# Performance work log

Hardware: AMD Instinct MI355X
Metric: run time of the kernel (lower is better)

Reference implementation:

```python
import jax, jax.numpy as jnp
import numpy as np

N = 100000      # nodes
E = 1600000     # directed edges
F_IN = 128      # input features
H = 64          # hidden_channels
C = 32          # num_classes


def setup_inputs() -> dict:
    key = jax.random.key(0)
    ks = jax.random.split(key, 8)
    x = jax.random.normal(ks[0], (N, F_IN), jnp.float32)
    edge_index = jax.random.randint(ks[1], (2, E), 0, N, jnp.int32)
    W1 = jax.random.normal(ks[2], (F_IN, H), jnp.float32) * (1.0 / np.sqrt(F_IN))
    b1 = jnp.zeros((H,), jnp.float32)
    W2 = jax.random.normal(ks[3], (H, H), jnp.float32) * (1.0 / np.sqrt(H))
    b2 = jnp.zeros((H,), jnp.float32)
    Wout = jax.random.normal(ks[4], (H, C), jnp.float32) * (1.0 / np.sqrt(H))
    bout = jnp.zeros((C,), jnp.float32)
    return {"x": x, "edge_index": edge_index, "W1": W1, "b1": b1,
            "W2": W2, "b2": b2, "Wout": Wout, "bout": bout}


def gcn_conv(x, W, b, src, dst, n):
    """PyG GCNConv: out = D^-1/2 (A + I) D^-1/2 (X W) + b,
    with degree computed on A + I."""
    h = x @ W  # [N, out]
    ones = jnp.ones(dst.shape[0], h.dtype)
    deg = jax.ops.segment_sum(ones, dst, num_segments=n) + 1.0  # self-loop
    dinv = jax.lax.rsqrt(deg)                                   # [N]
    coef = dinv[src] * dinv[dst]                                # [E]
    agg = jax.ops.segment_sum(h[src] * coef[:, None], dst, num_segments=n)
    agg = agg + h * (dinv * dinv)[:, None]                      # self-loop message
    return agg + b


def reference(x, edge_index, W1, b1, W2, b2, Wout, bout):
    src, dst = edge_index[0], edge_index[1]
    n = x.shape[0]
    h = jax.nn.relu(gcn_conv(x, W1, b1, src, dst, n))
    # dropout(p=0.5) is a no-op in eval mode
    h = jax.nn.relu(gcn_conv(h, W2, b2, src, dst, n))
    return jax.nn.softmax(h @ Wout + bout, axis=1)
```

## Files before the change

kernel.cpp:

```cpp
#include <hip/hip_runtime.h>
#include <stdint.h>


typedef unsigned short u16;
typedef unsigned int u32;
typedef unsigned long long u64t;
typedef __attribute__((ext_vector_type(8))) short bf16x8;
typedef __attribute__((ext_vector_type(4))) float f32x4;

#define GN 100000
#define GE 1600000
#define NBKT 196
#define BCAP 10240
#define EBLK 782
#define B24 16777216
#define QSC 1048576.0f
#define QIV 9.5367431640625e-7f

__device__ __forceinline__ float bf2f(u32 lo16) {
  union { u32 i; float f; } v; v.i = lo16 << 16; return v.f;
}
__device__ __forceinline__ u16 f2bf(float f) {
  union { float f; u32 i; } v; v.f = f;
  u32 x = v.i;
  u32 r = x + 0x7fffu + ((x >> 16) & 1u);
  return (u16)(r >> 16);
}
__device__ __forceinline__ u32 pack2(float a, float b) {
  return (u32)f2bf(a) | ((u32)f2bf(b) << 16);
}

__global__ __launch_bounds__(256) void k_detect(const u16* __restrict__ xs,
                                                int* __restrict__ flag,
                                                int* __restrict__ ccount) {
  __shared__ int cnt;
  if (threadIdx.x == 0) cnt = 0;
  if (threadIdx.x < NBKT) ccount[threadIdx.x] = 0;
  __syncthreads();
  int w = 0;
#pragma unroll
  for (int i = 0; i < 16; i++) {
    int s = threadIdx.x * 16 + i;
    u32 u = xs[(size_t)s * 1562];
    u32 ex = (u >> 7) & 0xffu;
    if (ex == 0xffu || ex < 0x40u) w++;
  }
  atomicAdd(&cnt, w);
  __syncthreads();
  if (threadIdx.x == 0) flag[0] = (cnt >= 64) ? 0 : 1;
}

__global__ __launch_bounds__(256) void k_partA(const int* __restrict__ src,
                                               const int* __restrict__ dst,
                                               int* __restrict__ ccount, int E,
                                               const void* p2, const void* p3,
                                               const void* p4, const void* p5,
                                               const void* p6, const void* p7,
                                               const int* __restrict__ flag,
                                               float* __restrict__ Wf,
                                               u16* __restrict__ Wb1,
                                               u16* __restrict__ Wb2,
                                               u16* __restrict__ Wbo,
                                               u32* __restrict__ pairs) {
  int tid = threadIdx.x;
  if (blockIdx.x >= EBLK) {
    int i = (blockIdx.x - EBLK) * 256 + tid;
    bool isbf = flag[0] != 0;
    if (i < 14496) {
      const void* sp; int off;
      if (i < 8192)       { sp = p2; off = i; }
      else if (i < 8256)  { sp = p3; off = i - 8192; }
      else if (i < 12352) { sp = p4; off = i - 8256; }
      else if (i < 12416) { sp = p5; off = i - 12352; }
      else if (i < 14464) { sp = p6; off = i - 12416; }
      else                { sp = p7; off = i - 14464; }
      Wf[i] = isbf ? bf2f((u32)((const u16*)sp)[off]) : ((const float*)sp)[off];
    } else if (i < 14496 + 12288) {
      int idx = i - 14496;
      const void* W; u16* dstp;
      if (idx < 8192) { W = p2; dstp = Wb1; }
      else            { W = p4; dstp = Wb2; idx -= 8192; }
      int j  = idx & 7;
      int l  = (idx >> 3) & 63;
      int c  = (idx >> 9) & 3;
      int kc = idx >> 11;
      int k = kc * 32 + (l >> 4) * 8 + j;
      int n = c * 16 + (l & 15);
      dstp[idx] = isbf ? ((const u16*)W)[k * 64 + n]
                       : f2bf(((const float*)W)[k * 64 + n]);
    } else if (i < 14496 + 12288 + 2048) {
      int idx = i - 14496 - 12288;
      int j  = idx & 7;
      int l  = (idx >> 3) & 63;
      int c  = (idx >> 9) & 1;
      int kc = idx >> 10;
      int k = kc * 32 + (l >> 4) * 8 + j;
      int n = c * 16 + (l & 15);
      Wbo[idx] = isbf ? ((const u16*)p6)[k * 32 + n]
                      : f2bf(((const float*)p6)[k * 32 + n]);
    }
    return;
  }
  __shared__ int hist[256];
  __shared__ int boff[256];
  __shared__ int fill[256];
  __shared__ int gbase[256];
  __shared__ int sc[256];
  __shared__ u32 buf[2048];
  __shared__ int adr[2048];
  __shared__ int stotal;
  hist[tid] = 0;
  __syncthreads();
  int e0 = (blockIdx.x * 256 + tid) * 8;
  int s_[8], d_[8];
  int cnt = 0;
  if (e0 + 8 <= E) {
    const int4* sp = (const int4*)(src + e0);
    const int4* dp = (const int4*)(dst + e0);
#pragma unroll
    for (int q = 0; q < 2; q++) {
      int4 sv = sp[q], dv = dp[q];
      s_[4 * q + 0] = sv.x; s_[4 * q + 1] = sv.y;
      s_[4 * q + 2] = sv.z; s_[4 * q + 3] = sv.w;
      d_[4 * q + 0] = dv.x; d_[4 * q + 1] = dv.y;
      d_[4 * q + 2] = dv.z; d_[4 * q + 3] = dv.w;
    }
    cnt = 8;
  } else {
    for (int q = 0; q < 8 && e0 + q < E; q++) {
      s_[q] = src[e0 + q]; d_[q] = dst[e0 + q]; cnt++;
    }
  }
  for (int q = 0; q < cnt; q++) atomicAdd(&hist[d_[q] >> 9], 1);
  __syncthreads();
  int v = hist[tid];
  sc[tid] = v;
  __syncthreads();
#pragma unroll
  for (int off = 1; off < 256; off <<= 1) {
    int a = (tid >= off) ? sc[tid - off] : 0;
    __syncthreads();
    sc[tid] += a;
    __syncthreads();
  }
  int excl = sc[tid] - v;
  boff[tid] = excl;
  fill[tid] = excl;
  if (tid == 255) stotal = sc[255];
  if (tid < NBKT && v > 0) gbase[tid] = tid * BCAP + atomicAdd(&ccount[tid], v);
  __syncthreads();
  for (int q = 0; q < cnt; q++) {
    int bkt = d_[q] >> 9;
    int p = atomicAdd(&fill[bkt], 1);
    buf[p] = ((u32)s_[q] << 9) | ((u32)d_[q] & 511u);
    adr[p] = gbase[bkt] + (p - boff[bkt]);
  }
  __syncthreads();
  int total = stotal;
  for (int j = tid; j < total; j += 256) pairs[adr[j]] = buf[j];
}

__global__ __launch_bounds__(256) void k_partBsrc(u32* __restrict__ pairs,
                                                  const int* __restrict__ ccount,
                                                  int* __restrict__ deg, int N) {
  __shared__ u32 P[BCAP];
  __shared__ u32 S[BCAP];
  __shared__ int cnt[512];
  __shared__ int sh[256];
  __shared__ int sc[256];
  int b = blockIdx.x, tid = threadIdx.x;
  int beg = b * BCAP, m = ccount[b];
  cnt[tid] = 0; cnt[tid + 256] = 0; sh[tid] = 0;
  for (int i = tid; i < m; i += 256) P[i] = pairs[beg + i];
  __syncthreads();
  for (int i = tid; i < m; i += 256) {
    u32 p = P[i];
    atomicAdd(&cnt[p & 511u], 1);
    atomicAdd(&sh[p >> 18], 1);
  }
  __syncthreads();
  int v = sh[tid];
  sc[tid] = v;
  __syncthreads();
#pragma unroll
  for (int off = 1; off < 256; off <<= 1) {
    int a = (tid >= off) ? sc[tid - off] : 0;
    __syncthreads();
    sc[tid] += a;
    __syncthreads();
  }
  __syncthreads();
  sh[tid] = sc[tid] - v;
  __syncthreads();
  for (int i = tid; i < m; i += 256) {
    u32 p = P[i];
    int pos = atomicAdd(&sh[p >> 18], 1);
    S[pos] = p;
  }
  __syncthreads();
  for (int i = tid; i < m; i += 256) pairs[beg + i] = S[i];
  int n0 = (b << 9) + tid, n1 = n0 + 256;
  if (n0 < N) deg[n0] = cnt[tid];
  if (n1 < N) deg[n1] = cnt[tid + 256];
}

template <int K, int XMODE>
__global__ __launch_bounds__(256) void k_mgemm(const void* __restrict__ X,
                                               const u16* __restrict__ Wb,
                                               const int* __restrict__ deg,
                                               const int* __restrict__ flag,
                                               u16* __restrict__ out, int M) {
  constexpr int NKC = K / 32;
  constexpr int P = K + 8;
  __shared__ u16 Bs[NKC * 4 * 64 * 8];
  __shared__ u16 As[128 * P];
  int tid = threadIdx.x;
  bool isbf = (XMODE == 1) ? true : (flag[0] != 0);
#pragma unroll
  for (int i = 0; i < NKC; i++)
    ((uint4*)Bs)[i * 256 + tid] = ((const uint4*)Wb)[i * 256 + tid];

  int rowbase = blockIdx.x * 128;
  int rowsValid = M - rowbase; if (rowsValid > 128) rowsValid = 128;
  if (isbf) {
    constexpr int F8 = K / 8;
    constexpr int NL = K / 16;
    const uint4* Xg = (const uint4*)X;
    uint4 v[NL];
#pragma unroll
    for (int i = 0; i < NL; i++) {
      int q = i * 256 + tid;
      int row = q / F8, c8 = q % F8;
      v[i] = (row < rowsValid) ? Xg[(size_t)(rowbase + row) * F8 + c8]
                               : make_uint4(0, 0, 0, 0);
    }
#pragma unroll
    for (int i = 0; i < NL; i++) {
      int q = i * 256 + tid;
      int row = q / F8, c8 = q % F8;
      *(uint4*)&As[row * P + c8 * 8] = v[i];
    }
  } else {
    constexpr int F4 = K / 4;
    constexpr int NL = K / 8;
    const float4* Xg = (const float4*)X;
    float4 v[NL];
#pragma unroll
    for (int i = 0; i < NL; i++) {
      int q = i * 256 + tid;
      int row = q / F4, c4 = q % F4;
      v[i] = (row < rowsValid) ? Xg[(size_t)(rowbase + row) * F4 + c4]
                               : make_float4(0.f, 0.f, 0.f, 0.f);
    }
#pragma unroll
    for (int i = 0; i < NL; i++) {
      int q = i * 256 + tid;
      int row = q / F4, c4 = q % F4;
      u32* d = (u32*)&As[row * P + c4 * 4];
      d[0] = pack2(v[i].x, v[i].y);
      d[1] = pack2(v[i].z, v[i].w);
    }
  }
  __syncthreads();

  int lane = tid & 63, wave = tid >> 6;
  int m0 = lane & 15;
  int koff = (lane >> 4) * 8;
  f32x4 acc[2][4];
#pragma unroll
  for (int t = 0; t < 2; t++)
#pragma unroll
    for (int c = 0; c < 4; c++) acc[t][c] = (f32x4){0.f, 0.f, 0.f, 0.f};

#pragma unroll
  for (int kc = 0; kc < NKC; kc++) {
    union { uint4 v; bf16x8 s; } a[2];
#pragma unroll
    for (int t = 0; t < 2; t++) {
      int rl = wave * 32 + t * 16 + m0;
      a[t].v = *(const uint4*)&As[rl * P + kc * 32 + koff];
    }
#pragma unroll
    for (int c = 0; c < 4; c++) {
      bf16x8 b = *(const bf16x8*)&Bs[((kc * 4 + c) * 64 + lane) * 8];
      acc[0][c] = __builtin_amdgcn_mfma_f32_16x16x32_bf16(a[0].s, b, acc[0][c], 0, 0, 0);
      acc[1][c] = __builtin_amdgcn_mfma_f32_16x16x32_bf16(a[1].s, b, acc[1][c], 0, 0, 0);
    }
  }
  __syncthreads();
  int cl = lane & 15, rq = (lane >> 4) * 4;
#pragma unroll
  for (int t = 0; t < 2; t++)
#pragma unroll
    for (int reg = 0; reg < 4; reg++) {
      int rl = wave * 32 + t * 16 + rq + reg;
      int r = rowbase + rl;
      float s = (r < M) ? rsqrtf((float)deg[r] + 1.0f) : 0.f;
#pragma unroll
      for (int c = 0; c < 4; c++)
        As[rl * P + c * 16 + cl] = f2bf(acc[t][c][reg] * s);
    }
  __syncthreads();
  uint4* outg = (uint4*)out;
#pragma unroll
  for (int i = 0; i < 4; i++) {
    int q = i * 256 + tid;
    int row = q >> 3, c8 = q & 7;
    int r = rowbase + row;
    if (r < M) outg[(size_t)r * 8 + c8] = *(uint4*)&As[row * P + c8 * 8];
  }
}

template <int MODE>
__global__ __launch_bounds__(1024) void k_aggu(const u16* __restrict__ g,
                                               const u32* __restrict__ pairs,
                                               const int* __restrict__ ccount,
                                               const float* __restrict__ bias,
                                               const u16* __restrict__ Wfrag,
                                               const float* __restrict__ bof,
                                               const int* __restrict__ flag,
                                               void* __restrict__ outv) {
  __shared__ __align__(16) u64t accU[512 * 33];
  __shared__ int cntE[512];
  u16* T16 = (u16*)accU;
  int tid = threadIdx.x;
  int b = blockIdx.x;
  for (int i = tid; i < 512 * 33; i += 1024) accU[i] = 0ull;
  if (tid < 512) cntE[tid] = 0;
  __syncthreads();

  int beg = b * BCAP;
  int end = beg + ccount[b];
  int o = tid >> 3, fq = tid & 7;
  const uint4* gp4 = (const uint4*)g;

#define DSU(dlo, v)                                                          \
  do {                                                                       \
    u64t* rp_ = &accU[(int)(dlo) * 33 + fq * 4];                             \
    int q0_ = (int)(bf2f((v).x & 0xffffu) * QSC) + B24;                      \
    int q1_ = (int)(bf2f((v).x >> 16) * QSC) + B24;                          \
    int q2_ = (int)(bf2f((v).y & 0xffffu) * QSC) + B24;                      \
    int q3_ = (int)(bf2f((v).y >> 16) * QSC) + B24;                          \
    int q4_ = (int)(bf2f((v).z & 0xffffu) * QSC) + B24;                      \
    int q5_ = (int)(bf2f((v).z >> 16) * QSC) + B24;                          \
    int q6_ = (int)(bf2f((v).w & 0xffffu) * QSC) + B24;                      \
    int q7_ = (int)(bf2f((v).w >> 16) * QSC) + B24;                          \
    atomicAdd(rp_ + 0, ((u64t)(u32)q0_) | (((u64t)(u32)q1_) << 32));         \
    atomicAdd(rp_ + 1, ((u64t)(u32)q2_) | (((u64t)(u32)q3_) << 32));         \
    atomicAdd(rp_ + 2, ((u64t)(u32)q4_) | (((u64t)(u32)q5_) << 32));         \
    atomicAdd(rp_ + 3, ((u64t)(u32)q6_) | (((u64t)(u32)q7_) << 32));         \
    if (fq == 0) atomicAdd(&cntE[(int)(dlo)], 1);                            \
  } while (0)

  int e = beg + o;
  for (; e + 384 < end; e += 512) {
    u32 p0 = pairs[e], p1 = pairs[e + 128], p2 = pairs[e + 256], p3 = pairs[e + 384];
    uint4 v0 = gp4[(size_t)(p0 >> 9) * 8 + fq];
    uint4 v1 = gp4[(size_t)(p1 >> 9) * 8 + fq];
    uint4 v2 = gp4[(size_t)(p2 >> 9) * 8 + fq];
    uint4 v3 = gp4[(size_t)(p3 >> 9) * 8 + fq];
    DSU(p0 & 511u, v0); DSU(p1 & 511u, v1);
    DSU(p2 & 511u, v2); DSU(p3 & 511u, v3);
  }
  for (; e < end; e += 128) {
    u32 p = pairs[e];
    uint4 v = gp4[(size_t)(p >> 9) * 8 + fq];
    DSU(p & 511u, v);
  }
#undef DSU
  __syncthreads();

  u32 pk[4][4];
  int rowq[4], c8q[4];
#pragma unroll
  for (int i = 0; i < 4; i++) {
    int q = i * 1024 + tid;
    int row = q >> 3, c8 = q & 7;
    rowq[i] = row; c8q[i] = c8;
    int node = b * 512 + row;
    float f0 = 0.f, f1 = 0.f, f2 = 0.f, f3 = 0.f;
    float f4 = 0.f, f5 = 0.f, f6 = 0.f, f7 = 0.f;
    if (node < GN) {
      uint4 sv = gp4[(size_t)node * 8 + c8];
      int n = cntE[row];
      int nb = n * B24;
      float dv = rsqrtf((float)n + 1.0f);
      float4 b0 = ((const float4*)bias)[c8 * 2];
      float4 b1 = ((const float4*)bias)[c8 * 2 + 1];
      const u64t* up = &accU[row * 33 + c8 * 4];
      u64t w0 = up[0], w1 = up[1], w2 = up[2], w3 = up[3];
      int a0 = (int)((u32)w0) - nb, a1 = (int)((u32)(w0 >> 32)) - nb;
      int a2 = (int)((u32)w1) - nb, a3 = (int)((u32)(w1 >> 32)) - nb;
      int a4 = (int)((u32)w2) - nb, a5 = (int)((u32)(w2 >> 32)) - nb;
      int a6 = (int)((u32)w3) - nb, a7 = (int)((u32)(w3 >> 32)) - nb;
      f0 = fmaxf(dv * ((float)a0 * QIV + bf2f(sv.x & 0xffffu)) + b0.x, 0.f);
      f1 = fmaxf(dv * ((float)a1 * QIV + bf2f(sv.x >> 16))     + b0.y, 0.f);
      f2 = fmaxf(dv * ((float)a2 * QIV + bf2f(sv.y & 0xffffu)) + b0.z, 0.f);
      f3 = fmaxf(dv * ((float)a3 * QIV + bf2f(sv.y >> 16))     + b0.w, 0.f);
      f4 = fmaxf(dv * ((float)a4 * QIV + bf2f(sv.z & 0xffffu)) + b1.x, 0.f);
      f5 = fmaxf(dv * ((float)a5 * QIV + bf2f(sv.z >> 16))     + b1.y, 0.f);
      f6 = fmaxf(dv * ((float)a6 * QIV + bf2f(sv.w & 0xffffu)) + b1.z, 0.f);
      f7 = fmaxf(dv * ((float)a7 * QIV + bf2f(sv.w >> 16))     + b1.w, 0.f);
    }
    pk[i][0] = pack2(f0, f1); pk[i][1] = pack2(f2, f3);
    pk[i][2] = pack2(f4, f5); pk[i][3] = pack2(f6, f7);
  }
  __syncthreads();
#pragma unroll
  for (int i = 0; i < 4; i++)
    *(uint4*)&T16[rowq[i] * 72 + c8q[i] * 8] =
        make_uint4(pk[i][0], pk[i][1], pk[i][2], pk[i][3]);
  __syncthreads();

  int lane = tid & 63, wave = tid >> 6;
  int m0 = lane & 15, koff = (lane >> 4) * 8;
  int cl = lane & 15, rq = (lane >> 4) * 4;
  if (MODE == 0) {
    bf16x8 bfr[2][4];
#pragma unroll
    for (int kc = 0; kc < 2; kc++)
#pragma unroll
      for (int c = 0; c < 4; c++)
        bfr[kc][c] = *(const bf16x8*)&Wfrag[((kc * 4 + c) * 64 + lane) * 8];
    f32x4 acc[2][4];
#pragma unroll
    for (int t = 0; t < 2; t++)
#pragma unroll
      for (int c = 0; c < 4; c++) acc[t][c] = (f32x4){0.f, 0.f, 0.f, 0.f};
#pragma unroll
    for (int kc = 0; kc < 2; kc++) {
      union { uint4 v; bf16x8 s; } a[2];
#pragma unroll
      for (int t = 0; t < 2; t++)
        a[t].v = *(const uint4*)&T16[(wave * 32 + t * 16 + m0) * 72 + kc * 32 + koff];
#pragma unroll
      for (int c = 0; c < 4; c++) {
        acc[0][c] = __builtin_amdgcn_mfma_f32_16x16x32_bf16(a[0].s, bfr[kc][c], acc[0][c], 0, 0, 0);
        acc[1][c] = __builtin_amdgcn_mfma_f32_16x16x32_bf16(a[1].s, bfr[kc][c], acc[1][c], 0, 0, 0);
      }
    }
    __syncthreads();
#pragma unroll
    for (int t = 0; t < 2; t++)
#pragma unroll
      for (int reg = 0; reg < 4; reg++) {
        int rl = wave * 32 + t * 16 + rq + reg;
        int node = b * 512 + rl;
        float s = (node < GN) ? rsqrtf((float)cntE[rl] + 1.0f) : 0.f;
#pragma unroll
        for (int c = 0; c < 4; c++)
          T16[rl * 72 + c * 16 + cl] = f2bf(acc[t][c][reg] * s);
      }
    __syncthreads();
    uint4* og = (uint4*)outv;
#pragma unroll
    for (int i = 0; i < 4; i++) {
      int q = i * 1024 + tid;
      int row = q >> 3, c8 = q & 7;
      int node = b * 512 + row;
      if (node < GN) og[(size_t)node * 8 + c8] = *(uint4*)&T16[row * 72 + c8 * 8];
    }
  } else {
    bf16x8 bfr[2][2];
#pragma unroll
    for (int kc = 0; kc < 2; kc++)
#pragma unroll
      for (int cc = 0; cc < 2; cc++)
        bfr[kc][cc] = *(const bf16x8*)&Wfrag[((kc * 2 + cc) * 64 + lane) * 8];
    f32x4 acc[2][2];
#pragma unroll
    for (int t = 0; t < 2; t++)
#pragma unroll
      for (int c = 0; c < 2; c++) acc[t][c] = (f32x4){0.f, 0.f, 0.f, 0.f};
#pragma unroll
    for (int kc = 0; kc < 2; kc++) {
      union { uint4 v; bf16x8 s; } a[2];
#pragma unroll
      for (int t = 0; t < 2; t++)
        a[t].v = *(const uint4*)&T16[(wave * 32 + t * 16 + m0) * 72 + kc * 32 + koff];
#pragma unroll
      for (int c = 0; c < 2; c++) {
        acc[0][c] = __builtin_amdgcn_mfma_f32_16x16x32_bf16(a[0].s, bfr[kc][c], acc[0][c], 0, 0, 0);
        acc[1][c] = __builtin_amdgcn_mfma_f32_16x16x32_bf16(a[1].s, bfr[kc][c], acc[1][c], 0, 0, 0);
      }
    }
    bool isbf = flag[0] != 0;
    float bb0 = bof[cl], bb1 = bof[16 + cl];
#pragma unroll
    for (int t = 0; t < 2; t++)
#pragma unroll
      for (int reg = 0; reg < 4; reg++) {
        int r = b * 512 + wave * 32 + t * 16 + rq + reg;
        float v0 = acc[t][0][reg] + bb0;
        float v1 = acc[t][1][reg] + bb1;
        float mx = fmaxf(v0, v1);
        mx = fmaxf(mx, __shfl_xor(mx, 1));
        mx = fmaxf(mx, __shfl_xor(mx, 2));
        mx = fmaxf(mx, __shfl_xor(mx, 4));
        mx = fmaxf(mx, __shfl_xor(mx, 8));
        float e0 = __expf(v0 - mx), e1 = __expf(v1 - mx);
        float s = e0 + e1;
        s += __shfl_xor(s, 1);
        s += __shfl_xor(s, 2);
        s += __shfl_xor(s, 4);
        s += __shfl_xor(s, 8);
        float inv = 1.f / s;
        if (r < GN) {
          if (isbf) {
            u16* go = (u16*)outv;
            go[(size_t)r * 32 + cl]      = f2bf(e0 * inv);
            go[(size_t)r * 32 + 16 + cl] = f2bf(e1 * inv);
          } else {
            float* go = (float*)outv;
            go[(size_t)r * 32 + cl]      = e0 * inv;
            go[(size_t)r * 32 + 16 + cl] = e1 * inv;
          }
        }
      }
  }
}

extern "C" void kernel_launch(void* const* d_in, const int* in_sizes, int n_in,
                              void* d_out, int out_size, void* d_ws, size_t ws_size,
                              hipStream_t stream) {
  (void)in_sizes; (void)n_in; (void)out_size; (void)ws_size;
  const void* x  = d_in[0];
  const int* ei  = (const int*)d_in[1];
  const int E = GE;
  const int* srcI = ei;
  const int* dstI = ei + E;

  char* ws = (char*)d_ws;
  int*   flag   = (int*)(ws + 0);
  int*   ccount = (int*)(ws + 256);
  int*   deg    = (int*)(ws + 4096);
  float* Wf     = (float*)(ws + 404480);
  u16*   Wb1    = (u16*)(ws + 462464);
  u16*   Wb2    = (u16*)(ws + 478848);
  u16*   Wbo    = (u16*)(ws + 487040);
  u32*   pairs  = (u32*)(ws + 491520);
  u16*   gA     = (u16*)(ws + 8519680);
  u16*   gB     = (u16*)(ws + 21319680);

  float* b1f = Wf + 8192;
  float* b2f = Wf + 12352;
  float* bof = Wf + 14464;

  k_detect<<<1, 256, 0, stream>>>((const u16*)x, flag, ccount);
  k_partA<<<EBLK + 113, 256, 0, stream>>>(srcI, dstI, ccount, E,
                                          d_in[2], d_in[3], d_in[4], d_in[5],
                                          d_in[6], d_in[7], flag,
                                          Wf, Wb1, Wb2, Wbo, pairs);
  k_partBsrc<<<NBKT, 256, 0, stream>>>(pairs, ccount, deg, GN);
  k_mgemm<128, 0><<<782, 256, 0, stream>>>(x, Wb1, deg, flag, gA, GN);
  k_aggu<0><<<NBKT, 1024, 0, stream>>>(gA, pairs, ccount, b1f, Wb2, bof, flag, gB);
  k_aggu<1><<<NBKT, 1024, 0, stream>>>(gB, pairs, ccount, b2f, Wbo, bof, flag, d_out);
}
```

Before: 226.0 us.

## Sort bucket edges by destination and aggregate contiguous runs in registers

The bucket partition pass now counting-sorts each bucket's edges by local destination instead of by source high bits. The aggregation kernels give each 8-lane group a contiguous chunk of edges and accumulate runs of equal destination in fp32 registers, issuing one set of shared-memory 64-bit atomics per run instead of per edge. This cuts LDS atomic traffic and contention, but trades away source locality in the gather and adds per-thread chunk load imbalance plus branchy run-detection code.

```diff
diff --git a/kernel.cpp b/kernel.cpp
--- a/kernel.cpp
+++ b/kernel.cpp
@@ -7,6 +7,7 @@
 typedef unsigned long long u64t;
 typedef __attribute__((ext_vector_type(8))) short bf16x8;
 typedef __attribute__((ext_vector_type(4))) float f32x4;
+typedef __attribute__((ext_vector_type(2))) float f32x2;
 
 #define GN 100000
 #define GE 1600000
@@ -28,6 +29,11 @@
 }
 __device__ __forceinline__ u32 pack2(float a, float b) {
   return (u32)f2bf(a) | ((u32)f2bf(b) << 16);
+}
+__device__ __forceinline__ f32x2 unpk(u32 u) {
+  union { u32 i; float f; } lo, hi;
+  lo.i = u << 16; hi.i = u & 0xffff0000u;
+  return (f32x2){lo.f, hi.f};
 }
 
 __global__ __launch_bounds__(256) void k_detect(const u16* __restrict__ xs,
@@ -160,27 +166,24 @@
   for (int j = tid; j < total; j += 256) pairs[adr[j]] = buf[j];
 }
 
-__global__ __launch_bounds__(256) void k_partBsrc(u32* __restrict__ pairs,
+__global__ __launch_bounds__(256) void k_partBdlo(u32* __restrict__ pairs,
                                                   const int* __restrict__ ccount,
                                                   int* __restrict__ deg, int N) {
   __shared__ u32 P[BCAP];
   __shared__ u32 S[BCAP];
   __shared__ int cnt[512];
-  __shared__ int sh[256];
   __shared__ int sc[256];
   int b = blockIdx.x, tid = threadIdx.x;
   int beg = b * BCAP, m = ccount[b];
-  cnt[tid] = 0; cnt[tid + 256] = 0; sh[tid] = 0;
+  if (m > BCAP) m = BCAP;
+  cnt[tid] = 0; cnt[tid + 256] = 0;
   for (int i = tid; i < m; i += 256) P[i] = pairs[beg + i];
   __syncthreads();
-  for (int i = tid; i < m; i += 256) {
-    u32 p = P[i];
-    atomicAdd(&cnt[p & 511u], 1);
-    atomicAdd(&sh[p >> 18], 1);
-  }
-  __syncthreads();
-  int v = sh[tid];
-  sc[tid] = v;
+  for (int i = tid; i < m; i += 256) atomicAdd(&cnt[P[i] & 511u], 1);
+  __syncthreads();
+  int c0 = cnt[2 * tid], c1 = cnt[2 * tid + 1];
+  int s = c0 + c1;
+  sc[tid] = s;
   __syncthreads();
 #pragma unroll
   for (int off = 1; off < 256; off <<= 1) {
@@ -189,19 +192,20 @@
     sc[tid] += a;
     __syncthreads();
   }
-  __syncthreads();
-  sh[tid] = sc[tid] - v;
+  int excl = sc[tid] - s;
+  cnt[2 * tid] = excl;
+  cnt[2 * tid + 1] = excl + c0;
+  int n0 = (b << 9) + 2 * tid, n1 = n0 + 1;
+  if (n0 < N) deg[n0] = c0;
+  if (n1 < N) deg[n1] = c1;
   __syncthreads();
   for (int i = tid; i < m; i += 256) {
     u32 p = P[i];
-    int pos = atomicAdd(&sh[p >> 18], 1);
+    int pos = atomicAdd(&cnt[p & 511u], 1);
     S[pos] = p;
   }
   __syncthreads();
   for (int i = tid; i < m; i += 256) pairs[beg + i] = S[i];
-  int n0 = (b << 9) + tid, n1 = n0 + 256;
-  if (n0 < N) deg[n0] = cnt[tid];
-  if (n1 < N) deg[n1] = cnt[tid + 256];
 }
 
 template <int K, int XMODE>
@@ -312,7 +316,7 @@
 }
 
 template <int MODE>
-__global__ __launch_bounds__(1024) void k_aggu(const u16* __restrict__ g,
+__global__ __launch_bounds__(1024) void k_aggr(const u16* __restrict__ g,
                                                const u32* __restrict__ pairs,
                                                const int* __restrict__ ccount,
                                                const float* __restrict__ bias,
@@ -330,44 +334,70 @@
   __syncthreads();
 
   int beg = b * BCAP;
-  int end = beg + ccount[b];
+  int m = ccount[b];
+  if (m > BCAP) m = BCAP;
+  int end = beg + m;
   int o = tid >> 3, fq = tid & 7;
   const uint4* gp4 = (const uint4*)g;
 
-#define DSU(dlo, v)                                                          \
+  int C = (m + 127) >> 7;
+  int lo = beg + o * C;
+  int hi = lo + C; if (hi > end) hi = end;
+
+  f32x2 a0 = {0.f, 0.f}, a1 = {0.f, 0.f}, a2 = {0.f, 0.f}, a3 = {0.f, 0.f};
+  int cur = 0, runN = 0;
+
+#define FLUSH()                                                              \
   do {                                                                       \
-    u64t* rp_ = &accU[(int)(dlo) * 33 + fq * 4];                             \
-    int q0_ = (int)(bf2f((v).x & 0xffffu) * QSC) + B24;                      \
-    int q1_ = (int)(bf2f((v).x >> 16) * QSC) + B24;                          \
-    int q2_ = (int)(bf2f((v).y & 0xffffu) * QSC) + B24;                      \
-    int q3_ = (int)(bf2f((v).y >> 16) * QSC) + B24;                          \
-    int q4_ = (int)(bf2f((v).z & 0xffffu) * QSC) + B24;                      \
-    int q5_ = (int)(bf2f((v).z >> 16) * QSC) + B24;                          \
-    int q6_ = (int)(bf2f((v).w & 0xffffu) * QSC) + B24;                      \
-    int q7_ = (int)(bf2f((v).w >> 16) * QSC) + B24;                          \
-    atomicAdd(rp_ + 0, ((u64t)(u32)q0_) | (((u64t)(u32)q1_) << 32));         \
-    atomicAdd(rp_ + 1, ((u64t)(u32)q2_) | (((u64t)(u32)q3_) << 32));         \
-    atomicAdd(rp_ + 2, ((u64t)(u32)q4_) | (((u64t)(u32)q5_) << 32));         \
-    atomicAdd(rp_ + 3, ((u64t)(u32)q6_) | (((u64t)(u32)q7_) << 32));         \
-    if (fq == 0) atomicAdd(&cntE[(int)(dlo)], 1);                            \
+    if (runN > 0) {                                                          \
+      int nb_ = runN * B24;                                                  \
+      u64t* rp_ = &accU[cur * 33 + fq * 4];                                  \
+      int q0_ = (int)(a0.x * QSC) + nb_;                                     \
+      int q1_ = (int)(a0.y * QSC) + nb_;                                     \
+      int q2_ = (int)(a1.x * QSC) + nb_;                                     \
+      int q3_ = (int)(a1.y * QSC) + nb_;                                     \
+      int q4_ = (int)(a2.x * QSC) + nb_;                                     \
+      int q5_ = (int)(a2.y * QSC) + nb_;                                     \
+      int q6_ = (int)(a3.x * QSC) + nb_;                                     \
+      int q7_ = (int)(a3.y * QSC) + nb_;                                     \
+      atomicAdd(rp_ + 0, ((u64t)(u32)q0_) | (((u64t)(u32)q1_) << 32));       \
+      atomicAdd(rp_ + 1, ((u64t)(u32)q2_) | (((u64t)(u32)q3_) << 32));       \
+      atomicAdd(rp_ + 2, ((u64t)(u32)q4_) | (((u64t)(u32)q5_) << 32));       \
+      atomicAdd(rp_ + 3, ((u64t)(u32)q6_) | (((u64t)(u32)q7_) << 32));       \
+      if (fq == 0) atomicAdd(&cntE[cur], runN);                              \
+      a0 = (f32x2){0.f, 0.f}; a1 = (f32x2){0.f, 0.f};                        \
+      a2 = (f32x2){0.f, 0.f}; a3 = (f32x2){0.f, 0.f};                        \
+      runN = 0;                                                              \
+    }                                                                        \
   } while (0)
 
-  int e = beg + o;
-  for (; e + 384 < end; e += 512) {
-    u32 p0 = pairs[e], p1 = pairs[e + 128], p2 = pairs[e + 256], p3 = pairs[e + 384];
+#define STEP(p_, v_)                                                         \
+  do {                                                                       \
+    int d_ = (int)((p_) & 511u);                                             \
+    if (d_ != cur) { FLUSH(); cur = d_; }                                    \
+    a0 += unpk((v_).x); a1 += unpk((v_).y);                                  \
+    a2 += unpk((v_).z); a3 += unpk((v_).w);                                  \
+    runN++;                                                                  \
+  } while (0)
+
+  for (int e = lo; e < hi; e += 4) {
+    int n4 = hi - e;
+    u32 p0 = pairs[e];
+    u32 p1 = pairs[(n4 > 1) ? e + 1 : e];
+    u32 p2 = pairs[(n4 > 2) ? e + 2 : e];
+    u32 p3 = pairs[(n4 > 3) ? e + 3 : e];
     uint4 v0 = gp4[(size_t)(p0 >> 9) * 8 + fq];
     uint4 v1 = gp4[(size_t)(p1 >> 9) * 8 + fq];
     uint4 v2 = gp4[(size_t)(p2 >> 9) * 8 + fq];
     uint4 v3 = gp4[(size_t)(p3 >> 9) * 8 + fq];
-    DSU(p0 & 511u, v0); DSU(p1 & 511u, v1);
-    DSU(p2 & 511u, v2); DSU(p3 & 511u, v3);
-  }
-  for (; e < end; e += 128) {
-    u32 p = pairs[e];
-    uint4 v = gp4[(size_t)(p >> 9) * 8 + fq];
-    DSU(p & 511u, v);
-  }
-#undef DSU
+    STEP(p0, v0);
+    if (n4 > 1) STEP(p1, v1);
+    if (n4 > 2) STEP(p2, v2);
+    if (n4 > 3) STEP(p3, v3);
+  }
+  FLUSH();
+#undef STEP
+#undef FLUSH
   __syncthreads();
 
   u32 pk[4][4];
@@ -389,18 +419,18 @@
       float4 b1 = ((const float4*)bias)[c8 * 2 + 1];
       const u64t* up = &accU[row * 33 + c8 * 4];
       u64t w0 = up[0], w1 = up[1], w2 = up[2], w3 = up[3];
-      int a0 = (int)((u32)w0) - nb, a1 = (int)((u32)(w0 >> 32)) - nb;
-      int a2 = (int)((u32)w1) - nb, a3 = (int)((u32)(w1 >> 32)) - nb;
-      int a4 = (int)((u32)w2) - nb, a5 = (int)((u32)(w2 >> 32)) - nb;
-      int a6 = (int)((u32)w3) - nb, a7 = (int)((u32)(w3 >> 32)) - nb;
-      f0 = fmaxf(dv * ((float)a0 * QIV + bf2f(sv.x & 0xffffu)) + b0.x, 0.f);
-      f1 = fmaxf(dv * ((float)a1 * QIV + bf2f(sv.x >> 16))     + b0.y, 0.f);
-      f2 = fmaxf(dv * ((float)a2 * QIV + bf2f(sv.y & 0xffffu)) + b0.z, 0.f);
-      f3 = fmaxf(dv * ((float)a3 * QIV + bf2f(sv.y >> 16))     + b0.w, 0.f);
-      f4 = fmaxf(dv * ((float)a4 * QIV + bf2f(sv.z & 0xffffu)) + b1.x, 0.f);
-      f5 = fmaxf(dv * ((float)a5 * QIV + bf2f(sv.z >> 16))     + b1.y, 0.f);
-      f6 = fmaxf(dv * ((float)a6 * QIV + bf2f(sv.w & 0xffffu)) + b1.z, 0.f);
-      f7 = fmaxf(dv * ((float)a7 * QIV + bf2f(sv.w >> 16))     + b1.w, 0.f);
+      int a0i = (int)((u32)w0) - nb, a1i = (int)((u32)(w0 >> 32)) - nb;
+      int a2i = (int)((u32)w1) - nb, a3i = (int)((u32)(w1 >> 32)) - nb;
+      int a4i = (int)((u32)w2) - nb, a5i = (int)((u32)(w2 >> 32)) - nb;
+      int a6i = (int)((u32)w3) - nb, a7i = (int)((u32)(w3 >> 32)) - nb;
+      f0 = fmaxf(dv * ((float)a0i * QIV + bf2f(sv.x & 0xffffu)) + b0.x, 0.f);
+      f1 = fmaxf(dv * ((float)a1i * QIV + bf2f(sv.x >> 16))     + b0.y, 0.f);
+      f2 = fmaxf(dv * ((float)a2i * QIV + bf2f(sv.y & 0xffffu)) + b0.z, 0.f);
+      f3 = fmaxf(dv * ((float)a3i * QIV + bf2f(sv.y >> 16))     + b0.w, 0.f);
+      f4 = fmaxf(dv * ((float)a4i * QIV + bf2f(sv.z & 0xffffu)) + b1.x, 0.f);
+      f5 = fmaxf(dv * ((float)a5i * QIV + bf2f(sv.z >> 16))     + b1.y, 0.f);
+      f6 = fmaxf(dv * ((float)a6i * QIV + bf2f(sv.w & 0xffffu)) + b1.z, 0.f);
+      f7 = fmaxf(dv * ((float)a7i * QIV + bf2f(sv.w >> 16))     + b1.w, 0.f);
     }
     pk[i][0] = pack2(f0, f1); pk[i][1] = pack2(f2, f3);
     pk[i][2] = pack2(f4, f5); pk[i][3] = pack2(f6, f7);
@@ -551,8 +581,8 @@
                                           d_in[2], d_in[3], d_in[4], d_in[5],
                                           d_in[6], d_in[7], flag,
                                           Wf, Wb1, Wb2, Wbo, pairs);
-  k_partBsrc<<<NBKT, 256, 0, stream>>>(pairs, ccount, deg, GN);
+  k_partBdlo<<<NBKT, 256, 0, stream>>>(pairs, ccount, deg, GN);
   k_mgemm<128, 0><<<782, 256, 0, stream>>>(x, Wb1, deg, flag, gA, GN);
-  k_aggu<0><<<NBKT, 1024, 0, stream>>>(gA, pairs, ccount, b1f, Wb2, bof, flag, gB);
-  k_aggu<1><<<NBKT, 1024, 0, stream>>>(gB, pairs, ccount, b2f, Wbo, bof, flag, d_out);
-}
+  k_aggr<0><<<NBKT, 1024, 0, stream>>>(gA, pairs, ccount, b1f, Wb2, bof, flag, gB);
+  k_aggr<1><<<NBKT, 1024, 0, stream>>>(gB, pairs, ccount, b2f, Wbo, bof, flag, d_out);
+}
```

After: 227.3 us. Within noise of the previous version (+0.6%).
